# Performance work log

Measured on AMD Instinct MI355X. Metric: run time of the kernel, lower is better.

## Reference

```python
import jax, jax.numpy as jnp
import numpy as np

B, S, D, H = 2, 2048, 512, 8
E = D // H  # per-head depth = 64


def setup_inputs() -> dict:
    key = jax.random.key(0)
    ks = jax.random.split(key, 10)
    x = jax.random.normal(ks[0], (B, S, D), dtype=jnp.float32)
    # binary mask: 1 = masked position (added as -1e9)
    attention_mask = jax.random.randint(ks[1], (B, S, S), 0, 2, dtype=jnp.int32)
    # per-head Dense weights stacked: [H, D, E] (Keras Dense: y = x @ W + b)
    sc = 1.0 / np.sqrt(D)
    Wq = jax.random.normal(ks[2], (H, D, E), dtype=jnp.float32) * sc
    Wk = jax.random.normal(ks[3], (H, D, E), dtype=jnp.float32) * sc
    Wv = jax.random.normal(ks[4], (H, D, E), dtype=jnp.float32) * sc
    bq = jnp.zeros((H, E), dtype=jnp.float32)
    bk = jnp.zeros((H, E), dtype=jnp.float32)
    bv = jnp.zeros((H, E), dtype=jnp.float32)
    Wo = jax.random.normal(ks[5], (D, D), dtype=jnp.float32) * sc
    bo = jnp.zeros((D,), dtype=jnp.float32)
    return {"x": x, "attention_mask": attention_mask, "Wq": Wq, "bq": bq,
            "Wk": Wk, "bk": bk, "Wv": Wv, "bv": bv, "Wo": Wo, "bo": bo}


def reference(x, attention_mask, Wq, bq, Wk, bk, Wv, bv, Wo, bo):
    # Per-head Dense projections, vectorized over heads: [B,H,S,E]
    q = jnp.einsum('bsd,hde->bhse', x, Wq) + bq[None, :, None, :]
    k = jnp.einsum('bsd,hde->bhse', x, Wk) + bk[None, :, None, :]
    v = jnp.einsum('bsd,hde->bhse', x, Wv) + bv[None, :, None, :]
    # scaled dot-product attention
    scores = jnp.einsum('bhse,bhte->bhst', q, k) / jnp.sqrt(jnp.float32(E))
    scores = scores + (-1e9) * attention_mask.astype(jnp.float32)[:, None, :, :]
    weights = jax.nn.softmax(scores, axis=-1)
    o = jnp.einsum('bhst,bhte->bhse', weights, v)
    # concat heads (head i -> columns [i*E:(i+1)*E]) then output Dense
    o = o.transpose(0, 2, 1, 3).reshape(B, S, D)
    return o @ Wo + bo
```

## Files before the change

kernel.cpp:

```cpp
#include <hip/hip_runtime.h>
#include <hip/hip_bf16.h>

typedef unsigned short u16;
typedef unsigned int u32;
typedef unsigned long long u64;
typedef short s16x8 __attribute__((ext_vector_type(8)));
typedef float f32x4 __attribute__((ext_vector_type(4)));
typedef float f32x16 __attribute__((ext_vector_type(16)));
typedef int i32x4 __attribute__((ext_vector_type(4)));

static __device__ __forceinline__ u16 f2b(float f) {
    union { float f; unsigned u; } x; x.f = f;
    unsigned r = x.u + 0x7fffu + ((x.u >> 16) & 1u);
    return (u16)(r >> 16);
}

static __device__ __forceinline__ u32 pkbf2(float a, float b) {
    union { __hip_bfloat162 h; u32 u; } c;
    c.h = __float22bfloat162_rn(make_float2(a, b));
    return c.u;
}

static __device__ __forceinline__ f32x16 zero16() {
    f32x16 z;
#pragma unroll
    for (int i = 0; i < 16; i++) z[i] = 0.f;
    return z;
}

static __device__ __forceinline__ s16x8 mk8(u32 a, u32 b, u32 c, u32 d) {
    union { u32 u[4]; s16x8 v; } x;
    x.u[0] = a; x.u[1] = b; x.u[2] = c; x.u[3] = d;
    return x.v;
}

static __device__ __forceinline__ u32 sx32(u32 v) {
    return (u32)__shfl_xor((int)v, 32, 64);
}

static __device__ __forceinline__ void gll16(const u16* g, u16* l) {
    __builtin_amdgcn_global_load_lds(
        (const __attribute__((address_space(1))) u32*)g,
        (__attribute__((address_space(3))) u32*)l, 16, 0, 0);
}


__global__ __launch_bounds__(256)
void k_pack_all(const float* __restrict__ x, const int* __restrict__ mask,
                const float* __restrict__ Wq, const float* __restrict__ Wk,
                const float* __restrict__ Wv, const float* __restrict__ Wo,
                const float* __restrict__ bq, const float* __restrict__ bk,
                const float* __restrict__ bv, const float* __restrict__ bo,
                u16* __restrict__ xb, u16* __restrict__ WT, u16* __restrict__ WoT,
                float* __restrict__ bias, u32* __restrict__ mb) {
    int idx = blockIdx.x * 256 + threadIdx.x;
    if (idx < 524288) {
        int i = idx * 4;
        float4 v = *(const float4*)(x + i);
        ushort4 o;
        o.x = f2b(v.x); o.y = f2b(v.y); o.z = f2b(v.z); o.w = f2b(v.w);
        *(ushort4*)(xb + i) = o;
    } else if (idx < 1310720) {
        int t = idx - 524288;
        int z = t >> 18, r = t & 262143;
        const float* W = (z == 0) ? Wq : (z == 1) ? Wk : Wv;
        int n = r >> 9, d = r & 511;
        WT[t] = f2b(W[((n >> 6) * 512 + d) * 64 + (n & 63)]);
    } else if (idx < 1572864) {
        int r = idx - 1310720;
        int n = r >> 9, d = r & 511;
        WoT[r] = f2b(Wo[d * 512 + n]);
    } else if (idx < 1574912) {
        int i = idx - 1572864;
        float v;
        if (i < 512) v = bq[i];
        else if (i < 1024) v = bk[i - 512];
        else if (i < 1536) v = bv[i - 1024];
        else v = bo[i - 1536];
        bias[i] = v;
    } else {
        int i2 = idx - 1574912;
        const int* p = mask + (size_t)i2 * 32;
        unsigned wv2 = 0;
#pragma unroll
        for (int j = 0; j < 32; j += 4) {
            int4 v = *(const int4*)(p + j);
            wv2 |= ((unsigned)(v.x & 1) << j) | ((unsigned)(v.y & 1) << (j + 1)) |
                   ((unsigned)(v.z & 1) << (j + 2)) | ((unsigned)(v.w & 1) << (j + 3));
        }
        mb[i2] = wv2;
    }
}


template<int MF, bool F32OUT>
__global__ __launch_bounds__(256)
void k_gemm(const u16* __restrict__ A, const u16* __restrict__ BTbase,
            const float* __restrict__ biasBase,
            u16* __restrict__ Cb, u16* __restrict__ Vt, float* __restrict__ Cf) {
    const int BM = MF * 32;
    const int nblk = blockIdx.x, mblk = blockIdx.y, z = blockIdx.z;
    const u16* BT = BTbase + (size_t)z * 262144;
    const float* bias = biasBase + z * 512;
    __shared__ __align__(16) u16 As[MF * 32 * 64];
    __shared__ __align__(16) u16 Bs[128 * 64];
    const int tid = threadIdx.x, lane = tid & 63, wv = tid >> 6;
    const int lr = lane & 15, lg = lane >> 4;
    const int wr = (wv >> 1) * (MF * 16), wc = (wv & 1) * 64;
    const u16* Ag = A + (size_t)(mblk * BM) * 512;
    const u16* Bg = BT + (size_t)(nblk * 128) * 512;

    f32x4 acc[MF][4];
#pragma unroll
    for (int i = 0; i < MF; i++)
#pragma unroll
        for (int j = 0; j < 4; j++) acc[i][j] = (f32x4){0.f, 0.f, 0.f, 0.f};

    for (int kt = 0; kt < 8; kt++) {
        __syncthreads();
#pragma unroll
        for (int i = 0; i < MF; i++) {
            int f = i * 256 + tid, r = f >> 3, c = f & 7;
            *(i32x4*)&As[r * 64 + ((c * 8) ^ ((r & 7) << 3))] =
                *(const i32x4*)(Ag + (size_t)r * 512 + kt * 64 + c * 8);
        }
#pragma unroll
        for (int i = 0; i < 4; i++) {
            int f = i * 256 + tid, r = f >> 3, c = f & 7;
            *(i32x4*)&Bs[r * 64 + ((c * 8) ^ ((r & 7) << 3))] =
                *(const i32x4*)(Bg + (size_t)r * 512 + kt * 64 + c * 8);
        }
        __syncthreads();
#pragma unroll
        for (int ks = 0; ks < 2; ks++) {
            s16x8 af[MF], bf[4];
#pragma unroll
            for (int mf = 0; mf < MF; mf++) {
                int r = wr + mf * 16 + lr;
                af[mf] = *(const s16x8*)&As[r * 64 + ((ks * 32 + lg * 8) ^ ((r & 7) << 3))];
            }
#pragma unroll
            for (int nf = 0; nf < 4; nf++) {
                int r = wc + nf * 16 + lr;
                bf[nf] = *(const s16x8*)&Bs[r * 64 + ((ks * 32 + lg * 8) ^ ((r & 7) << 3))];
            }
#pragma unroll
            for (int mf = 0; mf < MF; mf++)
#pragma unroll
                for (int nf = 0; nf < 4; nf++)
                    acc[mf][nf] = __builtin_amdgcn_mfma_f32_16x16x32_bf16(
                        af[mf], bf[nf], acc[mf][nf], 0, 0, 0);
        }
    }
#pragma unroll
    for (int nf = 0; nf < 4; nf++) {
        int col = nblk * 128 + wc + nf * 16 + lr;
        float bval = bias[col];
#pragma unroll
        for (int mf = 0; mf < MF; mf++) {
            int row0 = mblk * BM + wr + mf * 16 + lg * 4;
            if (F32OUT) {
#pragma unroll
                for (int r = 0; r < 4; r++)
                    Cf[(size_t)(row0 + r) * 512 + col] = acc[mf][nf][r] + bval;
            } else if (z == 2) {
                ushort4 o;
                o.x = f2b(acc[mf][nf][0] + bval);
                o.y = f2b(acc[mf][nf][1] + bval);
                o.z = f2b(acc[mf][nf][2] + bval);
                o.w = f2b(acc[mf][nf][3] + bval);
                *(ushort4*)(Vt + (size_t)(row0 >> 11) * 1048576 +
                            (size_t)col * 2048 + (row0 & 2047)) = o;
            } else {
#pragma unroll
                for (int r = 0; r < 4; r++)
                    Cb[(size_t)z * 2097152 + (size_t)(row0 + r) * 512 + col] =
                        f2b(acc[mf][nf][r] + bval);
            }
        }
    }
}


__global__ __launch_bounds__(512, 4)
void k_attn(const u16* __restrict__ qkv, const u16* __restrict__ vt,
            const u32* __restrict__ mb, u16* __restrict__ oc) {
    const int qt = blockIdx.x, h = blockIdx.y, b = blockIdx.z;
    const u16* Qb = qkv + (size_t)b * 1048576 + h * 64;
    const u16* Kb = Qb + 2097152;
    const u16* VtH = vt + (size_t)b * 1048576 + (size_t)h * 131072;

    __shared__ __align__(16) u16 SMEM[32768];
    __shared__ float mlbuf[8][32][2];
    __shared__ float rscbuf[8][32];

    const int tid = threadIdx.x;
    const int lane = tid & 63, w = tid >> 6;
    const int hi = lane >> 5, l31 = lane & 31;
    const int qg = w & 1, kvq = w >> 1;
    const int qrow = qt * 64 + qg * 32 + l31;

    const int lr8 = lane >> 3, lc8 = (lane & 7) ^ (lane >> 3);
    const u16* Ksrc0 = Kb + (size_t)(kvq * 512 + qg * 32 + lr8) * 512 + lc8 * 8;
    const u16* Vsrc0 = VtH + (size_t)(qg * 32 + lr8) * 2048 + kvq * 512 + lc8 * 8;
    u16* KqW = &SMEM[kvq * 8192 + qg * 2048];
    u16* VqW = &SMEM[kvq * 8192 + 4096 + qg * 2048];

    s16x8 qf[4];
#pragma unroll
    for (int ks = 0; ks < 4; ks++)
        qf[ks] = *(const s16x8*)(Qb + (size_t)qrow * 512 + ks * 16 + hi * 8);

#pragma unroll
    for (int i = 0; i < 4; i++) {
        gll16(Ksrc0 + (size_t)(i * 8) * 512, KqW + i * 512);
        gll16(Vsrc0 + (size_t)(i * 8) * 2048, VqW + i * 512);
    }
    const size_t mbase = ((size_t)b * 2048 + qrow) * 64 + kvq * 16;
    u64 mreg = *(const u64*)(mb + mbase);
    __syncthreads();

    f32x16 accO0 = zero16(), accO1 = zero16();
    f32x4 lvec = (f32x4){0.f, 0.f, 0.f, 0.f};
    float m_run = -3.0e38f;
    const float SC = 0.18033688011112042f;

    const u16* KH = &SMEM[kvq * 8192];
    const u16* VH = KH + 4096;
    const int swv = (l31 & 7) << 3;

    for (int t = 0; t < 8; t++) {
        u64 mnx = 0;
        if (t < 7) mnx = *(const u64*)(mb + mbase + (t + 1) * 2);

        f32x16 sa0 = zero16(), sa1 = zero16();
#pragma unroll
        for (int ks = 0; ks < 4; ks++) {
            const int cb = ks * 16 + hi * 8;
            s16x8 kf0 = *(const s16x8*)&KH[l31 * 64 + (cb ^ swv)];
            s16x8 kf1 = *(const s16x8*)&KH[(32 + l31) * 64 + (cb ^ swv)];
            sa0 = __builtin_amdgcn_mfma_f32_32x32x16_bf16(kf0, qf[ks], sa0, 0, 0, 0);
            sa1 = __builtin_amdgcn_mfma_f32_32x32x16_bf16(kf1, qf[ks], sa1, 0, 0, 0);
        }
        sa0 *= SC; sa1 *= SC;

        float pm;
        {
            float mx[8];
#pragma unroll
            for (int j = 0; j < 8; j++)
                mx[j] = fmaxf(fmaxf(sa0[j], sa0[j + 8]), fmaxf(sa1[j], sa1[j + 8]));
#pragma unroll
            for (int s = 4; s > 0; s >>= 1)
#pragma unroll
                for (int j = 0; j < s; j++) mx[j] = fmaxf(mx[j], mx[j + s]);
            pm = fmaxf(mx[0], __shfl_xor(mx[0], 32, 64));
        }

        if (__ballot(pm > m_run + 8.0f)) {
            float mn = fmaxf(m_run, pm);
            float rs = __builtin_amdgcn_exp2f(m_run - mn);
            m_run = mn;
            lvec *= rs;
            if (lane < 32) rscbuf[w][lane] = rs;
#pragma unroll
            for (int r = 0; r < 16; r++) {
                float rf = rscbuf[w][(r & 3) + 8 * (r >> 2) + 4 * hi];
                accO0[r] *= rf; accO1[r] *= rf;
            }
        }

        const u32 mw0 = ((u32)mreg) >> (hi * 4);
        const u32 mw1 = ((u32)(mreg >> 32)) >> (hi * 4);
        u32 pk0[8], pk1[8];
#pragma unroll
        for (int g = 0; g < 8; g++) {
            const int r0 = 2 * g, r1 = 2 * g + 1;
            const int p0 = (r0 & 3) + 8 * (r0 >> 2);
            const int p1 = (r1 & 3) + 8 * (r1 >> 2);
            float a = ((mw0 >> p0) & 1u) ? 0.f : __builtin_amdgcn_exp2f(sa0[r0] - m_run);
            float b2 = ((mw0 >> p1) & 1u) ? 0.f : __builtin_amdgcn_exp2f(sa0[r1] - m_run);
            float c = ((mw1 >> p0) & 1u) ? 0.f : __builtin_amdgcn_exp2f(sa1[r0] - m_run);
            float d = ((mw1 >> p1) & 1u) ? 0.f : __builtin_amdgcn_exp2f(sa1[r1] - m_run);
            lvec[r0 & 3] += a + c;
            lvec[r1 & 3] += b2 + d;
            pk0[g] = pkbf2(a, b2);
            pk1[g] = pkbf2(c, d);
        }

        s16x8 pa[4];
        {
            u32 x0 = sx32(pk0[0]), x1 = sx32(pk0[1]), x2 = sx32(pk0[2]), x3 = sx32(pk0[3]);
            u32 x4 = sx32(pk0[4]), x5 = sx32(pk0[5]), x6 = sx32(pk0[6]), x7 = sx32(pk0[7]);
            pa[0] = mk8(hi ? x2 : pk0[0], hi ? x3 : pk0[1],
                        hi ? pk0[2] : x0, hi ? pk0[3] : x1);
            pa[1] = mk8(hi ? x6 : pk0[4], hi ? x7 : pk0[5],
                        hi ? pk0[6] : x4, hi ? pk0[7] : x5);
        }
        {
            u32 x0 = sx32(pk1[0]), x1 = sx32(pk1[1]), x2 = sx32(pk1[2]), x3 = sx32(pk1[3]);
            u32 x4 = sx32(pk1[4]), x5 = sx32(pk1[5]), x6 = sx32(pk1[6]), x7 = sx32(pk1[7]);
            pa[2] = mk8(hi ? x2 : pk1[0], hi ? x3 : pk1[1],
                        hi ? pk1[2] : x0, hi ? pk1[3] : x1);
            pa[3] = mk8(hi ? x6 : pk1[4], hi ? x7 : pk1[5],
                        hi ? pk1[6] : x4, hi ? pk1[7] : x5);
        }

#pragma unroll
        for (int ksg = 0; ksg < 4; ksg++) {
            const int cb = ksg * 16 + hi * 8;
            s16x8 bv0 = *(const s16x8*)&VH[l31 * 64 + (cb ^ swv)];
            s16x8 bv1 = *(const s16x8*)&VH[(32 + l31) * 64 + (cb ^ swv)];
            accO0 = __builtin_amdgcn_mfma_f32_32x32x16_bf16(pa[ksg], bv0, accO0, 0, 0, 0);
            accO1 = __builtin_amdgcn_mfma_f32_32x32x16_bf16(pa[ksg], bv1, accO1, 0, 0, 0);
        }

        __syncthreads();
        if (t < 7) {
            const size_t ro = (size_t)(t + 1) * 64;
#pragma unroll
            for (int i = 0; i < 4; i++) {
                gll16(Ksrc0 + (ro + i * 8) * 512, KqW + i * 512);
                gll16(Vsrc0 + ro + (size_t)(i * 8) * 2048, VqW + i * 512);
            }
            mreg = mnx;
        }
        __syncthreads();
    }

    float Ls = (lvec[0] + lvec[1]) + (lvec[2] + lvec[3]);
    Ls += __shfl_xor(Ls, 32, 64);

    float* Obuf = (float*)SMEM;
    const int lx = (lane & 7) * 4;
    const int obase = w * 2048 + lane * 32;
#pragma unroll
    for (int g = 0; g < 4; g++) {
        *(f32x4*)&Obuf[obase + ((4 * g) ^ lx)] =
            (f32x4){accO0[4 * g], accO0[4 * g + 1], accO0[4 * g + 2], accO0[4 * g + 3]};
        *(f32x4*)&Obuf[obase + ((16 + 4 * g) ^ lx)] =
            (f32x4){accO1[4 * g], accO1[4 * g + 1], accO1[4 * g + 2], accO1[4 * g + 3]};
    }
    if (lane < 32) { mlbuf[w][lane][0] = m_run; mlbuf[w][lane][1] = Ls; }
    __syncthreads();

    const int qg2 = w & 1, rq = w >> 1;
    f32x4 v0[4], v1[4];
#pragma unroll
    for (int j = 0; j < 4; j++) {
        const int wp = qg2 + 2 * j;
        v0[j] = *(const f32x4*)&Obuf[wp * 2048 + lane * 32 + ((rq * 4) ^ lx)];
        v1[j] = *(const f32x4*)&Obuf[wp * 2048 + lane * 32 + ((16 + rq * 4) ^ lx)];
    }
#pragma unroll
    for (int k = 0; k < 4; k++) {
        const int q_k = k + 8 * rq + 4 * hi;
        float mj[4], Lj[4];
#pragma unroll
        for (int j = 0; j < 4; j++) {
            const int wp = qg2 + 2 * j;
            mj[j] = mlbuf[wp][q_k][0];
            Lj[j] = mlbuf[wp][q_k][1];
        }
        float M = fmaxf(fmaxf(mj[0], mj[1]), fmaxf(mj[2], mj[3]));
        float g0 = __builtin_amdgcn_exp2f(mj[0] - M);
        float g1 = __builtin_amdgcn_exp2f(mj[1] - M);
        float g2 = __builtin_amdgcn_exp2f(mj[2] - M);
        float g3 = __builtin_amdgcn_exp2f(mj[3] - M);
        float D = Lj[0] * g0 + Lj[1] * g1 + Lj[2] * g2 + Lj[3] * g3;
        float inv = 1.0f / D;
        float o0 = (g0 * v0[0][k] + g1 * v0[1][k] + g2 * v0[2][k] + g3 * v0[3][k]) * inv;
        float o1 = (g0 * v1[0][k] + g1 * v1[1][k] + g2 * v1[2][k] + g3 * v1[3][k]) * inv;
        const size_t orow = ((size_t)b * 2048 + qt * 64 + qg2 * 32 + q_k) * 512 + h * 64;
        oc[orow + l31]      = f2b(o0);
        oc[orow + 32 + l31] = f2b(o1);
    }
}


extern "C" void kernel_launch(void* const* d_in, const int* in_sizes, int n_in,
                              void* d_out, int out_size, void* d_ws, size_t ws_size,
                              hipStream_t stream) {
    const float* x    = (const float*)d_in[0];
    const int*   mask = (const int*)d_in[1];
    const float* Wq   = (const float*)d_in[2];
    const float* bq   = (const float*)d_in[3];
    const float* Wk   = (const float*)d_in[4];
    const float* bk   = (const float*)d_in[5];
    const float* Wv   = (const float*)d_in[6];
    const float* bv   = (const float*)d_in[7];
    const float* Wo   = (const float*)d_in[8];
    const float* bo   = (const float*)d_in[9];

    u16* xb     = (u16*)d_ws;
    u16* WT     = xb + 2097152;
    u16* WoT    = WT + 786432;
    u16* qkv    = WoT + 262144;
    u16* vtp    = qkv + 4194304;
    u16* oc     = qkv + 6291456;
    float* bias = (float*)(oc + 2097152);
    u32* mbits  = (u32*)(bias + 2048);

    k_pack_all<<<7176, 256, 0, stream>>>(x, mask, Wq, Wk, Wv, Wo, bq, bk, bv, bo,
                                         xb, WT, WoT, bias, mbits);
    k_gemm<2, false><<<dim3(4, 64, 3), 256, 0, stream>>>(xb, WT, bias, qkv, vtp, nullptr);
    k_attn<<<dim3(32, 8, 2), 512, 0, stream>>>(qkv, vtp, mbits, oc);
    k_gemm<2, true><<<dim3(4, 64, 1), 256, 0, stream>>>(oc, WoT, bias + 1536,
                                                        nullptr, nullptr, (float*)d_out);
}
```

Before: 82.88 us.

## Double-buffer K/V tiles with 32-key steps and one barrier per iteration

The attention loop now works on 32-key tiles over 16 iterations instead of 64-key tiles over 8. Shared memory is split into two buffers so the next tile's K/V async loads are issued before computing on the current one, which drops one of the two __syncthreads per iteration. The V tile uses a new swizzle for its narrower 32-column layout, and s_setprio is raised around MFMA blocks. The smaller tiles mean more loop iterations and less MFMA work per barrier, which may offset the gain from overlapping loads.

```diff
diff --git a/kernel.cpp b/kernel.cpp
--- a/kernel.cpp
+++ b/kernel.cpp
@@ -200,11 +200,10 @@
     const int qg = w & 1, kvq = w >> 1;
     const int qrow = qt * 64 + qg * 32 + l31;
 
-    const int lr8 = lane >> 3, lc8 = (lane & 7) ^ (lane >> 3);
-    const u16* Ksrc0 = Kb + (size_t)(kvq * 512 + qg * 32 + lr8) * 512 + lc8 * 8;
-    const u16* Vsrc0 = VtH + (size_t)(qg * 32 + lr8) * 2048 + kvq * 512 + lc8 * 8;
-    u16* KqW = &SMEM[kvq * 8192 + qg * 2048];
-    u16* VqW = &SMEM[kvq * 8192 + 4096 + qg * 2048];
+    const int lr8 = lane >> 3, lc8 = (lane & 7) ^ lr8;
+    const int vr16 = lane >> 2, vc4 = (lane & 3) ^ ((lane >> 3) & 3);
+    const int kvbase0 = kvq * 512;
+    const int qoff = kvq * 4096;
 
     s16x8 qf[4];
 #pragma unroll
@@ -212,44 +211,57 @@
         qf[ks] = *(const s16x8*)(Qb + (size_t)qrow * 512 + ks * 16 + hi * 8);
 
 #pragma unroll
-    for (int i = 0; i < 4; i++) {
-        gll16(Ksrc0 + (size_t)(i * 8) * 512, KqW + i * 512);
-        gll16(Vsrc0 + (size_t)(i * 8) * 2048, VqW + i * 512);
-    }
-    const size_t mbase = ((size_t)b * 2048 + qrow) * 64 + kvq * 16;
-    u64 mreg = *(const u64*)(mb + mbase);
+    for (int i = 0; i < 2; i++) {
+        gll16(Kb + (size_t)(kvbase0 + qg * 16 + i * 8 + lr8) * 512 + lc8 * 8,
+              &SMEM[qoff + (qg * 16 + i * 8) * 64]);
+        gll16(VtH + (size_t)(qg * 32 + i * 16 + vr16) * 2048 + kvbase0 + vc4 * 8,
+              &SMEM[qoff + 2048 + qg * 1024 + i * 512]);
+    }
+    const int mbase = (b * 2048 + qrow) * 64 + kvq * 16;
+    u32 mreg = mb[mbase];
     __syncthreads();
 
     f32x16 accO0 = zero16(), accO1 = zero16();
     f32x4 lvec = (f32x4){0.f, 0.f, 0.f, 0.f};
     float m_run = -3.0e38f;
     const float SC = 0.18033688011112042f;
-
-    const u16* KH = &SMEM[kvq * 8192];
-    const u16* VH = KH + 4096;
-    const int swv = (l31 & 7) << 3;
-
-    for (int t = 0; t < 8; t++) {
-        u64 mnx = 0;
-        if (t < 7) mnx = *(const u64*)(mb + mbase + (t + 1) * 2);
-
-        f32x16 sa0 = zero16(), sa1 = zero16();
+    const int kswz = (l31 & 7) << 3;
+    const int vkey = (l31 >> 1) & 3;
+
+    for (int t = 0; t < 16; t++) {
+        const int bo = (t & 1) << 14;
+        u32 mnx = 0;
+        if (t < 15) {
+            const int bn = bo ^ 16384;
+            const int kvb = kvbase0 + (t + 1) * 32;
+#pragma unroll
+            for (int i = 0; i < 2; i++) {
+                gll16(Kb + (size_t)(kvb + qg * 16 + i * 8 + lr8) * 512 + lc8 * 8,
+                      &SMEM[bn + qoff + (qg * 16 + i * 8) * 64]);
+                gll16(VtH + (size_t)(qg * 32 + i * 16 + vr16) * 2048 + kvb + vc4 * 8,
+                      &SMEM[bn + qoff + 2048 + qg * 1024 + i * 512]);
+            }
+            mnx = mb[mbase + t + 1];
+        }
+        const u16* Kq = &SMEM[bo + qoff];
+        const u16* Vq = &SMEM[bo + qoff + 2048];
+
+        f32x16 sa = zero16();
+        __builtin_amdgcn_s_setprio(1);
 #pragma unroll
         for (int ks = 0; ks < 4; ks++) {
             const int cb = ks * 16 + hi * 8;
-            s16x8 kf0 = *(const s16x8*)&KH[l31 * 64 + (cb ^ swv)];
-            s16x8 kf1 = *(const s16x8*)&KH[(32 + l31) * 64 + (cb ^ swv)];
-            sa0 = __builtin_amdgcn_mfma_f32_32x32x16_bf16(kf0, qf[ks], sa0, 0, 0, 0);
-            sa1 = __builtin_amdgcn_mfma_f32_32x32x16_bf16(kf1, qf[ks], sa1, 0, 0, 0);
-        }
-        sa0 *= SC; sa1 *= SC;
+            s16x8 kf = *(const s16x8*)&Kq[l31 * 64 + (cb ^ kswz)];
+            sa = __builtin_amdgcn_mfma_f32_32x32x16_bf16(kf, qf[ks], sa, 0, 0, 0);
+        }
+        __builtin_amdgcn_s_setprio(0);
+        sa *= SC;
 
         float pm;
         {
             float mx[8];
 #pragma unroll
-            for (int j = 0; j < 8; j++)
-                mx[j] = fmaxf(fmaxf(sa0[j], sa0[j + 8]), fmaxf(sa1[j], sa1[j + 8]));
+            for (int j = 0; j < 8; j++) mx[j] = fmaxf(sa[j], sa[j + 8]);
 #pragma unroll
             for (int s = 4; s > 0; s >>= 1)
 #pragma unroll
@@ -270,62 +282,43 @@
             }
         }
 
-        const u32 mw0 = ((u32)mreg) >> (hi * 4);
-        const u32 mw1 = ((u32)(mreg >> 32)) >> (hi * 4);
-        u32 pk0[8], pk1[8];
+        const u32 mw = mreg >> (hi * 4);
+        u32 pk[8];
 #pragma unroll
         for (int g = 0; g < 8; g++) {
             const int r0 = 2 * g, r1 = 2 * g + 1;
             const int p0 = (r0 & 3) + 8 * (r0 >> 2);
             const int p1 = (r1 & 3) + 8 * (r1 >> 2);
-            float a = ((mw0 >> p0) & 1u) ? 0.f : __builtin_amdgcn_exp2f(sa0[r0] - m_run);
-            float b2 = ((mw0 >> p1) & 1u) ? 0.f : __builtin_amdgcn_exp2f(sa0[r1] - m_run);
-            float c = ((mw1 >> p0) & 1u) ? 0.f : __builtin_amdgcn_exp2f(sa1[r0] - m_run);
-            float d = ((mw1 >> p1) & 1u) ? 0.f : __builtin_amdgcn_exp2f(sa1[r1] - m_run);
-            lvec[r0 & 3] += a + c;
-            lvec[r1 & 3] += b2 + d;
-            pk0[g] = pkbf2(a, b2);
-            pk1[g] = pkbf2(c, d);
-        }
-
-        s16x8 pa[4];
+            float a = ((mw >> p0) & 1u) ? 0.f : __builtin_amdgcn_exp2f(sa[r0] - m_run);
+            float b2 = ((mw >> p1) & 1u) ? 0.f : __builtin_amdgcn_exp2f(sa[r1] - m_run);
+            lvec[r0 & 3] += a;
+            lvec[r1 & 3] += b2;
+            pk[g] = pkbf2(a, b2);
+        }
+
+        s16x8 pa[2];
         {
-            u32 x0 = sx32(pk0[0]), x1 = sx32(pk0[1]), x2 = sx32(pk0[2]), x3 = sx32(pk0[3]);
-            u32 x4 = sx32(pk0[4]), x5 = sx32(pk0[5]), x6 = sx32(pk0[6]), x7 = sx32(pk0[7]);
-            pa[0] = mk8(hi ? x2 : pk0[0], hi ? x3 : pk0[1],
-                        hi ? pk0[2] : x0, hi ? pk0[3] : x1);
-            pa[1] = mk8(hi ? x6 : pk0[4], hi ? x7 : pk0[5],
-                        hi ? pk0[6] : x4, hi ? pk0[7] : x5);
-        }
-        {
-            u32 x0 = sx32(pk1[0]), x1 = sx32(pk1[1]), x2 = sx32(pk1[2]), x3 = sx32(pk1[3]);
-            u32 x4 = sx32(pk1[4]), x5 = sx32(pk1[5]), x6 = sx32(pk1[6]), x7 = sx32(pk1[7]);
-            pa[2] = mk8(hi ? x2 : pk1[0], hi ? x3 : pk1[1],
-                        hi ? pk1[2] : x0, hi ? pk1[3] : x1);
-            pa[3] = mk8(hi ? x6 : pk1[4], hi ? x7 : pk1[5],
-                        hi ? pk1[6] : x4, hi ? pk1[7] : x5);
-        }
-
-#pragma unroll
-        for (int ksg = 0; ksg < 4; ksg++) {
-            const int cb = ksg * 16 + hi * 8;
-            s16x8 bv0 = *(const s16x8*)&VH[l31 * 64 + (cb ^ swv)];
-            s16x8 bv1 = *(const s16x8*)&VH[(32 + l31) * 64 + (cb ^ swv)];
+            u32 x0 = sx32(pk[0]), x1 = sx32(pk[1]), x2 = sx32(pk[2]), x3 = sx32(pk[3]);
+            u32 x4 = sx32(pk[4]), x5 = sx32(pk[5]), x6 = sx32(pk[6]), x7 = sx32(pk[7]);
+            pa[0] = mk8(hi ? x2 : pk[0], hi ? x3 : pk[1],
+                        hi ? pk[2] : x0, hi ? pk[3] : x1);
+            pa[1] = mk8(hi ? x6 : pk[4], hi ? x7 : pk[5],
+                        hi ? pk[6] : x4, hi ? pk[7] : x5);
+        }
+
+        __builtin_amdgcn_s_setprio(1);
+#pragma unroll
+        for (int ksg = 0; ksg < 2; ksg++) {
+            const int off = ((ksg * 2 + hi) ^ vkey) << 3;
+            s16x8 bv0 = *(const s16x8*)&Vq[l31 * 32 + off];
+            s16x8 bv1 = *(const s16x8*)&Vq[(32 + l31) * 32 + off];
             accO0 = __builtin_amdgcn_mfma_f32_32x32x16_bf16(pa[ksg], bv0, accO0, 0, 0, 0);
             accO1 = __builtin_amdgcn_mfma_f32_32x32x16_bf16(pa[ksg], bv1, accO1, 0, 0, 0);
         }
+        __builtin_amdgcn_s_setprio(0);
 
         __syncthreads();
-        if (t < 7) {
-            const size_t ro = (size_t)(t + 1) * 64;
-#pragma unroll
-            for (int i = 0; i < 4; i++) {
-                gll16(Ksrc0 + (ro + i * 8) * 512, KqW + i * 512);
-                gll16(Vsrc0 + ro + (size_t)(i * 8) * 2048, VqW + i * 512);
-            }
-            mreg = mnx;
-        }
-        __syncthreads();
+        mreg = mnx;
     }
 
     float Ls = (lvec[0] + lvec[1]) + (lvec[2] + lvec[3]);
```

Result: no change. 83.45 us (+0.7%).
